# Performance work log

Hardware: AMD Instinct MI355X
Metric: run time of the kernel (lower is better)

## Reference

```python
import jax, jax.numpy as jnp
import numpy as np

N_NODES = 50000
N_EDGES = 1600000
IN_CH = 128
HID_CH = 128


def setup_inputs() -> dict:
    key = jax.random.key(0)
    ks = jax.random.split(key, 8)
    node_embed = jax.random.normal(ks[0], (N_NODES, IN_CH), dtype=jnp.float32)
    node_pos = jax.random.normal(ks[1], (N_NODES, 3), dtype=jnp.float32)
    edge_index = jax.random.randint(ks[2], (2, N_EDGES), 0, N_NODES, dtype=jnp.int64)
    # Linear weights stored as [in, out] so y = x @ W + b (matches torch x @ W.T + b)
    W_res = jax.random.normal(ks[3], (IN_CH, HID_CH), dtype=jnp.float32) / np.sqrt(IN_CH)
    W_msg = jax.random.normal(ks[4], (2 * IN_CH + 1, HID_CH), dtype=jnp.float32) / np.sqrt(2 * IN_CH + 1)
    b_msg = jax.random.normal(ks[5], (HID_CH,), dtype=jnp.float32) * 0.01
    W_upd = jax.random.normal(ks[6], (IN_CH + HID_CH, HID_CH), dtype=jnp.float32) / np.sqrt(IN_CH + HID_CH)
    b_upd = jax.random.normal(ks[7], (HID_CH,), dtype=jnp.float32) * 0.01
    return {"node_embed": node_embed, "node_pos": node_pos, "edge_index": edge_index,
            "W_res": W_res, "W_msg": W_msg, "b_msg": b_msg, "W_upd": W_upd, "b_upd": b_upd}


def reference(node_embed, node_pos, edge_index, W_res, W_msg, b_msg, W_upd, b_upd):
    row, col = edge_index[0], edge_index[1]
    # squared distance per edge: [E, 1]
    diff = node_pos[row] - node_pos[col]
    dist = jnp.sum(diff * diff, axis=1, keepdims=True)
    # message MLP on concat(src, tgt, dist): [E, 2*in+1] -> [E, hidden]
    msg_in = jnp.concatenate([node_embed[row], node_embed[col], dist], axis=-1)
    msg = jax.nn.relu(msg_in @ W_msg + b_msg)
    # scatter-sum messages into target nodes (index = col, as in original)
    aggr = jax.ops.segment_sum(msg, col, num_segments=N_NODES)
    upd_in = jnp.concatenate([node_embed, aggr], axis=-1)
    new_node_embed = node_embed @ W_res + jax.nn.relu(upd_in @ W_upd + b_upd)
    return new_node_embed
```

## Files before the change

kernel.cpp:

```cpp
#include <hip/hip_runtime.h>
#include <hip/hip_bf16.h>
#include <cstdint>


typedef __bf16 bf16x8 __attribute__((ext_vector_type(8)));
typedef float floatx4 __attribute__((ext_vector_type(4)));
typedef float floatx2 __attribute__((ext_vector_type(2)));
typedef unsigned int uintx4 __attribute__((ext_vector_type(4)));

#define BUCKET_CAP 128
#define NBINS 256
#define BIN_CAP 10240
#define PASS2_SPLIT 4

__device__ __forceinline__ ushort f2bf(float f) {
  union { float f; uint i; } v; v.f = f;
  uint r = v.i + 0x7fff + ((v.i >> 16) & 1);
  return (ushort)(r >> 16);
}
__device__ __forceinline__ bf16x8 load_frag(const ushort* p) {
  uint4 v = *(const uint4*)p;
  return __builtin_bit_cast(bf16x8, v);
}
__device__ __forceinline__ floatx2 pmax0(floatx2 a) {
#if __has_builtin(__builtin_elementwise_max)
  return __builtin_elementwise_max(a, (floatx2)(0.f));
#else
  floatx2 r; r.x = fmaxf(a.x, 0.f); r.y = fmaxf(a.y, 0.f); return r;
#endif
}

struct WSrc { const float* s[5]; };

__global__ __launch_bounds__(256) void k0_cast(
    const float* __restrict__ embed, ushort* __restrict__ Eb, int n4, int nb_cast,
    WSrc ws, ushort* __restrict__ Wt)
{
  if ((int)blockIdx.x < nb_cast) {
    int i = blockIdx.x * 256 + threadIdx.x;
    if (i < n4) {
      float4 v = ((const float4*)embed)[i];
      ushort4 o;
      o.x = f2bf(v.x); o.y = f2bf(v.y); o.z = f2bf(v.z); o.w = f2bf(v.w);
      ((ushort4*)Eb)[i] = o;
    }
    return;
  }
  int wb = blockIdx.x - nb_cast;
  const float* s = ws.s[wb];
  ushort* d = Wt + wb * 16384;
  for (int i = threadIdx.x; i < 16384; i += 256) {
    int k = i >> 7, n = i & 127;
    d[n * 128 + k] = f2bf(s[i]);
  }
}

__global__ __launch_bounds__(256) void k1_binpass(
    const int* __restrict__ ei, int E, const float* __restrict__ pos,
    uint* __restrict__ bin_cursor, uint2* __restrict__ binned)
{
  __shared__ uint hist[NBINS];
  __shared__ uint base[NBINS];
  __shared__ uint lcur[NBINS];
  const int t = threadIdx.x;
  hist[t] = 0;
  __syncthreads();

  const int e0 = blockIdx.x * 2048 + t * 8;
  int rr[8], cc[8];
  uint2 rec[8];
  bool any = (e0 < E);
  if (any) {
    int4 r0 = ((const int4*)(ei + e0))[0];
    int4 r1 = ((const int4*)(ei + e0))[1];
    int4 c0 = ((const int4*)(ei + E + e0))[0];
    int4 c1 = ((const int4*)(ei + E + e0))[1];
    rr[0]=r0.x; rr[1]=r0.y; rr[2]=r0.z; rr[3]=r0.w;
    rr[4]=r1.x; rr[5]=r1.y; rr[6]=r1.z; rr[7]=r1.w;
    cc[0]=c0.x; cc[1]=c0.y; cc[2]=c0.z; cc[3]=c0.w;
    cc[4]=c1.x; cc[5]=c1.y; cc[6]=c1.z; cc[7]=c1.w;
#pragma unroll
    for (int j = 0; j < 8; ++j) {
      bool val = (e0 + j < E);
      int r = val ? rr[j] : 0, c = val ? cc[j] : 0;
      float dx = pos[3 * r + 0] - pos[3 * c + 0];
      float dy = pos[3 * r + 1] - pos[3 * c + 1];
      float dz = pos[3 * r + 2] - pos[3 * c + 2];
      float dist = dx * dx + dy * dy + dz * dz;
      rec[j].x = ((uint)c << 16) | (uint)r;
      rec[j].y = (uint)f2bf(dist);
      if (val) atomicAdd(&hist[c >> 8], 1u);
    }
  }
  __syncthreads();
  uint h = hist[t];
  base[t] = h ? atomicAdd(bin_cursor + t, h) : 0u;
  lcur[t] = 0;
  __syncthreads();
  if (any) {
#pragma unroll
    for (int j = 0; j < 8; ++j) {
      if (e0 + j < E) {
        int b = cc[j] >> 8;
        uint ofs = atomicAdd(&lcur[b], 1u);
        uint idx = base[b] + ofs;
        if (idx < BIN_CAP)
          binned[(size_t)b * BIN_CAP + idx] = rec[j];
      }
    }
  }
}

__global__ __launch_bounds__(256) void k2_proj_pass2(
    const ushort* __restrict__ Ab, int M, int rt,
    const ushort* __restrict__ W1t, const ushort* __restrict__ W2t,
    const float* __restrict__ b_msg,
    unsigned char* __restrict__ P1, ushort* __restrict__ P2b,
    const uint* __restrict__ bin_cursor, const uint2* __restrict__ binned,
    int* __restrict__ counts, uint* __restrict__ recs)
{
  if ((int)blockIdx.x >= rt) {
    int b = blockIdx.x - rt;
    int bin = b / PASS2_SPLIT, part = b % PASS2_SPLIT;
    int cnt = (int)min(bin_cursor[bin], (uint)BIN_CAP);
    int s0 = (int)((long)cnt * part / PASS2_SPLIT);
    int s1 = (int)((long)cnt * (part + 1) / PASS2_SPLIT);
    const uint2* src = binned + (size_t)bin * BIN_CAP;
    for (int i = s0 + threadIdx.x; i < s1; i += 256) {
      uint2 rec = src[i];
      uint c = rec.x >> 16;
      int slot = atomicAdd(counts + c, 1);
      if (slot < BUCKET_CAP)
        recs[(size_t)c * BUCKET_CAP + slot] = (rec.x << 16) | (rec.y & 0xffffu);
    }
    return;
  }

  const int wv = threadIdx.x >> 6, lane = threadIdx.x & 63;
  const int q = lane >> 4, lr = lane & 15;
  const int m0 = blockIdx.x * 32;
  const int n0 = wv * 32;

  const ushort* Wt2[2] = {W1t, W2t};
  bf16x8 bfr[2][2][4];
#pragma unroll
  for (int ws = 0; ws < 2; ++ws)
#pragma unroll
    for (int nt = 0; nt < 2; ++nt) {
      int colc = n0 + nt * 16 + lr;
#pragma unroll
      for (int kc = 0; kc < 4; ++kc)
        bfr[ws][nt][kc] = load_frag(Wt2[ws] + colc * 128 + kc * 32 + q * 8);
    }

  floatx4 z = {0.f, 0.f, 0.f, 0.f};
  floatx4 acc[2][2][2];
#pragma unroll
  for (int ws = 0; ws < 2; ++ws)
#pragma unroll
    for (int mt = 0; mt < 2; ++mt)
#pragma unroll
      for (int nt = 0; nt < 2; ++nt) acc[ws][mt][nt] = z;

  const int r0 = min(m0 + lr, M - 1);
  const int r1 = min(m0 + 16 + lr, M - 1);
#pragma unroll
  for (int kc = 0; kc < 4; ++kc) {
    bf16x8 a0 = load_frag(Ab + (size_t)r0 * 128 + kc * 32 + q * 8);
    bf16x8 a1 = load_frag(Ab + (size_t)r1 * 128 + kc * 32 + q * 8);
#pragma unroll
    for (int ws = 0; ws < 2; ++ws)
#pragma unroll
      for (int nt = 0; nt < 2; ++nt) {
        acc[ws][0][nt] = __builtin_amdgcn_mfma_f32_16x16x32_bf16(a0, bfr[ws][nt][kc], acc[ws][0][nt], 0, 0, 0);
        acc[ws][1][nt] = __builtin_amdgcn_mfma_f32_16x16x32_bf16(a1, bfr[ws][nt][kc], acc[ws][1][nt], 0, 0, 0);
      }
  }

#pragma unroll
  for (int nt = 0; nt < 2; ++nt) {
    int colc = n0 + nt * 16 + lr;
    float bias = b_msg[colc];
#pragma unroll
    for (int mt = 0; mt < 2; ++mt)
#pragma unroll
      for (int i = 0; i < 4; ++i) {
        int r = m0 + mt * 16 + q * 4 + i;
        if (r < M) {
          int p8 = __builtin_amdgcn_cvt_pk_fp8_f32(acc[0][mt][nt][i], 0.f, 0, false);
          P1[(size_t)r * 128 + colc] = (unsigned char)(p8 & 0xff);
          P2b[(size_t)r * 128 + colc] = f2bf(acc[1][mt][nt][i] + bias);
        }
      }
  }
}

__global__ __launch_bounds__(256) void aggregate(const int* __restrict__ counts,
                                                 const uint* __restrict__ recs,
                                                 const unsigned char* __restrict__ P1,
                                                 const ushort* __restrict__ P2b,
                                                 const float* __restrict__ wd,
                                                 ushort* __restrict__ aggr, int M)
{
  int n = blockIdx.x * 4 + (threadIdx.x >> 6);
  if (n >= M) return;
  const int lane = threadIdx.x & 63;
  const int ch = lane * 2;

  float2 wl = *(const float2*)(wd + ch);
  floatx2 wv = {wl.x, wl.y};
  uint p2u = *(const uint*)(P2b + (size_t)n * 128 + ch);
  floatx2 p2 = {__int_as_float((int)(p2u << 16)),
                __int_as_float((int)(p2u & 0xffff0000u))};

  const int cnt = min(counts[n], BUCKET_CAP);
  const uint* base = recs + (size_t)n * BUCKET_CAP;
  floatx2 accA = {0.f, 0.f}, accB = {0.f, 0.f};

  auto edge = [&](uint rec, floatx2& acc) {
    float d = __int_as_float((int)(rec << 16));
    uint row = rec >> 16;
    ushort qu = *(const ushort*)(P1 + (size_t)row * 128 + ch);
    floatx2 qv = {__builtin_amdgcn_cvt_f32_fp8((int)qu, 0),
                  __builtin_amdgcn_cvt_f32_fp8((int)qu, 1)};
    floatx2 base2 = qv + p2;
#if __has_builtin(__builtin_elementwise_fma)
    floatx2 t = __builtin_elementwise_fma((floatx2)(d), wv, base2);
#else
    floatx2 t = (floatx2)(d) * wv + base2;
#endif
    acc += pmax0(t);
  };

  int i = 0;
  for (; i + 8 <= cnt; i += 8) {
    uintx4 ra = __builtin_nontemporal_load((const uintx4*)(base + i));
    uintx4 rb = __builtin_nontemporal_load((const uintx4*)(base + i + 4));
    edge(ra.x, accA); edge(ra.y, accB); edge(ra.z, accA); edge(ra.w, accB);
    edge(rb.x, accA); edge(rb.y, accB); edge(rb.z, accA); edge(rb.w, accB);
  }
  for (; i < cnt; ++i) edge(base[i], accA);

  floatx2 acc = accA + accB;
  uint o = (uint)f2bf(acc.x) | ((uint)f2bf(acc.y) << 16);
  *(uint*)(aggr + (size_t)n * 128 + ch) = o;
}

__global__ __launch_bounds__(256) void gemm_upd_mfma(
    const ushort* __restrict__ Eb, const ushort* __restrict__ Gb, int M,
    const ushort* __restrict__ Wu1t, const ushort* __restrict__ Wu2t,
    const ushort* __restrict__ Wrt, const float* __restrict__ b_upd,
    float* __restrict__ out)
{
  const int wv = threadIdx.x >> 6, lane = threadIdx.x & 63;
  const int q = lane >> 4, lr = lane & 15;
  const int m0 = blockIdx.x * 32;
  const int n0 = wv * 32;

  bf16x8 b1[2][4], b2[2][4], br[2][4];
#pragma unroll
  for (int nt = 0; nt < 2; ++nt) {
    int colc = n0 + nt * 16 + lr;
#pragma unroll
    for (int kc = 0; kc < 4; ++kc) {
      b1[nt][kc] = load_frag(Wu1t + colc * 128 + kc * 32 + q * 8);
      b2[nt][kc] = load_frag(Wu2t + colc * 128 + kc * 32 + q * 8);
      br[nt][kc] = load_frag(Wrt  + colc * 128 + kc * 32 + q * 8);
    }
  }

  floatx4 z = {0.f, 0.f, 0.f, 0.f};
  floatx4 acc_u[2][2], acc_r[2][2];
#pragma unroll
  for (int mt = 0; mt < 2; ++mt)
#pragma unroll
    for (int nt = 0; nt < 2; ++nt) { acc_u[mt][nt] = z; acc_r[mt][nt] = z; }

  const int r0 = min(m0 + lr, M - 1);
  const int r1 = min(m0 + 16 + lr, M - 1);
#pragma unroll
  for (int kc = 0; kc < 4; ++kc) {
    bf16x8 ae0 = load_frag(Eb + (size_t)r0 * 128 + kc * 32 + q * 8);
    bf16x8 ae1 = load_frag(Eb + (size_t)r1 * 128 + kc * 32 + q * 8);
    bf16x8 ag0 = load_frag(Gb + (size_t)r0 * 128 + kc * 32 + q * 8);
    bf16x8 ag1 = load_frag(Gb + (size_t)r1 * 128 + kc * 32 + q * 8);
#pragma unroll
    for (int nt = 0; nt < 2; ++nt) {
      acc_u[0][nt] = __builtin_amdgcn_mfma_f32_16x16x32_bf16(ae0, b1[nt][kc], acc_u[0][nt], 0, 0, 0);
      acc_u[1][nt] = __builtin_amdgcn_mfma_f32_16x16x32_bf16(ae1, b1[nt][kc], acc_u[1][nt], 0, 0, 0);
      acc_u[0][nt] = __builtin_amdgcn_mfma_f32_16x16x32_bf16(ag0, b2[nt][kc], acc_u[0][nt], 0, 0, 0);
      acc_u[1][nt] = __builtin_amdgcn_mfma_f32_16x16x32_bf16(ag1, b2[nt][kc], acc_u[1][nt], 0, 0, 0);
      acc_r[0][nt] = __builtin_amdgcn_mfma_f32_16x16x32_bf16(ae0, br[nt][kc], acc_r[0][nt], 0, 0, 0);
      acc_r[1][nt] = __builtin_amdgcn_mfma_f32_16x16x32_bf16(ae1, br[nt][kc], acc_r[1][nt], 0, 0, 0);
    }
  }

#pragma unroll
  for (int nt = 0; nt < 2; ++nt) {
    int colc = n0 + nt * 16 + lr;
    float bias = b_upd[colc];
#pragma unroll
    for (int mt = 0; mt < 2; ++mt)
#pragma unroll
      for (int i = 0; i < 4; ++i) {
        int r = m0 + mt * 16 + q * 4 + i;
        if (r < M)
          out[(size_t)r * 128 + colc] = acc_r[mt][nt][i] + fmaxf(acc_u[mt][nt][i] + bias, 0.f);
      }
  }
}

extern "C" void kernel_launch(void* const* d_in, const int* in_sizes, int n_in,
                              void* d_out, int out_size, void* d_ws, size_t ws_size,
                              hipStream_t stream)
{
  const float* embed = (const float*)d_in[0];
  const float* pos   = (const float*)d_in[1];
  const int*   ei    = (const int*)d_in[2];
  const float* W_res = (const float*)d_in[3];
  const float* W_msg = (const float*)d_in[4];
  const float* b_msg = (const float*)d_in[5];
  const float* W_upd = (const float*)d_in[6];
  const float* b_upd = (const float*)d_in[7];
  float* out = (float*)d_out;

  const int M = in_sizes[0] / 128;
  const int E = in_sizes[2] / 2;

  ushort* Eb = (ushort*)d_ws;
  unsigned char* P1f8 = (unsigned char*)(Eb + (size_t)M * 128);
  ushort* P2b = (ushort*)(P1f8 + (size_t)M * 128);
  ushort* Gb  = P2b + (size_t)M * 128;
  ushort* Wt  = Gb  + (size_t)M * 128;
  uint*   recs = (uint*)(Wt + 5 * 16384);
  uint2*  binned = (uint2*)(recs + (size_t)M * BUCKET_CAP);
  int*    counts = (int*)(binned + (size_t)NBINS * BIN_CAP);
  uint*   bin_cursor = (uint*)(counts + M);

  (void)hipMemsetAsync(counts, 0, (size_t)(M + NBINS) * sizeof(int), stream);

  WSrc wsrc;
  wsrc.s[0] = W_msg;
  wsrc.s[1] = W_msg + 128 * 128;
  wsrc.s[2] = W_res;
  wsrc.s[3] = W_upd;
  wsrc.s[4] = W_upd + 128 * 128;

  int n4 = M * 128 / 4;
  int nb_cast = (n4 + 255) / 256;
  k0_cast<<<nb_cast + 5, 256, 0, stream>>>(embed, Eb, n4, nb_cast, wsrc, Wt);

  int bb = (E + 2047) / 2048;
  k1_binpass<<<bb, 256, 0, stream>>>(ei, E, pos, bin_cursor, binned);

  int rt = (M + 31) / 32;
  k2_proj_pass2<<<rt + NBINS * PASS2_SPLIT, 256, 0, stream>>>(
      Eb, M, rt, Wt, Wt + 16384, b_msg, P1f8, P2b,
      bin_cursor, binned, counts, recs);

  aggregate<<<(M + 3) / 4, 256, 0, stream>>>(counts, recs, P1f8, P2b,
                                             W_msg + 256 * 128, Gb, M);

  gemm_upd_mfma<<<rt, 256, 0, stream>>>(Eb, Gb, M, Wt + 3 * 16384, Wt + 4 * 16384,
                                        Wt + 2 * 16384, b_upd, out);
}
```

Measured before the change: 283.4 us.

## Fuse cast and binning kernels; deepen aggregate unroll with packed fp8 convert

Merges the embedding/weight cast kernel and the edge binning pass into one launch, with block ranges selecting the role, so one kernel launch and its tail go away and the two independent stages can overlap. The aggregate loop now loads 32 records at a time into four accumulators, which gives more gather loads in flight. It also uses a packed fp8-to-f32 convert and computes the row offset with a single shift and mask. The trade-off is higher register pressure in aggregate, and the fused kernel now carries shared memory even for blocks that only cast.

```diff
diff --git a/kernel.cpp b/kernel.cpp
--- a/kernel.cpp
+++ b/kernel.cpp
@@ -29,39 +29,50 @@
   floatx2 r; r.x = fmaxf(a.x, 0.f); r.y = fmaxf(a.y, 0.f); return r;
 #endif
 }
+__device__ __forceinline__ floatx2 cvtpk2(uint qu) {
+#if __has_builtin(__builtin_amdgcn_cvt_pk_f32_fp8)
+  return __builtin_amdgcn_cvt_pk_f32_fp8((int)qu, false);
+#else
+  floatx2 o = {__builtin_amdgcn_cvt_f32_fp8((int)qu, 0),
+               __builtin_amdgcn_cvt_f32_fp8((int)qu, 1)};
+  return o;
+#endif
+}
 
 struct WSrc { const float* s[5]; };
 
-__global__ __launch_bounds__(256) void k0_cast(
+__global__ __launch_bounds__(256) void k01_cast_bin(
     const float* __restrict__ embed, ushort* __restrict__ Eb, int n4, int nb_cast,
-    WSrc ws, ushort* __restrict__ Wt)
-{
-  if ((int)blockIdx.x < nb_cast) {
-    int i = blockIdx.x * 256 + threadIdx.x;
-    if (i < n4) {
-      float4 v = ((const float4*)embed)[i];
-      ushort4 o;
-      o.x = f2bf(v.x); o.y = f2bf(v.y); o.z = f2bf(v.z); o.w = f2bf(v.w);
-      ((ushort4*)Eb)[i] = o;
+    WSrc ws, ushort* __restrict__ Wt,
+    const int* __restrict__ ei, int E, const float* __restrict__ pos,
+    uint* __restrict__ bin_cursor, uint2* __restrict__ binned, int bb)
+{
+  __shared__ uint hist[NBINS];
+  __shared__ uint sbase[NBINS];
+  __shared__ uint lcur[NBINS];
+
+  if ((int)blockIdx.x >= bb) {
+    int cb = blockIdx.x - bb;
+    if (cb < nb_cast) {
+      int i = cb * 256 + threadIdx.x;
+      if (i < n4) {
+        float4 v = ((const float4*)embed)[i];
+        ushort4 o;
+        o.x = f2bf(v.x); o.y = f2bf(v.y); o.z = f2bf(v.z); o.w = f2bf(v.w);
+        ((ushort4*)Eb)[i] = o;
+      }
+      return;
+    }
+    int wb = cb - nb_cast;
+    const float* s = ws.s[wb];
+    ushort* d = Wt + wb * 16384;
+    for (int i = threadIdx.x; i < 16384; i += 256) {
+      int k = i >> 7, n = i & 127;
+      d[n * 128 + k] = f2bf(s[i]);
     }
     return;
   }
-  int wb = blockIdx.x - nb_cast;
-  const float* s = ws.s[wb];
-  ushort* d = Wt + wb * 16384;
-  for (int i = threadIdx.x; i < 16384; i += 256) {
-    int k = i >> 7, n = i & 127;
-    d[n * 128 + k] = f2bf(s[i]);
-  }
-}
-
-__global__ __launch_bounds__(256) void k1_binpass(
-    const int* __restrict__ ei, int E, const float* __restrict__ pos,
-    uint* __restrict__ bin_cursor, uint2* __restrict__ binned)
-{
-  __shared__ uint hist[NBINS];
-  __shared__ uint base[NBINS];
-  __shared__ uint lcur[NBINS];
+
   const int t = threadIdx.x;
   hist[t] = 0;
   __syncthreads();
@@ -94,7 +105,7 @@
   }
   __syncthreads();
   uint h = hist[t];
-  base[t] = h ? atomicAdd(bin_cursor + t, h) : 0u;
+  sbase[t] = h ? atomicAdd(bin_cursor + t, h) : 0u;
   lcur[t] = 0;
   __syncthreads();
   if (any) {
@@ -103,7 +114,7 @@
       if (e0 + j < E) {
         int b = cc[j] >> 8;
         uint ofs = atomicAdd(&lcur[b], 1u);
-        uint idx = base[b] + ofs;
+        uint idx = sbase[b] + ofs;
         if (idx < BIN_CAP)
           binned[(size_t)b * BIN_CAP + idx] = rec[j];
       }
@@ -215,33 +226,53 @@
 
   const int cnt = min(counts[n], BUCKET_CAP);
   const uint* base = recs + (size_t)n * BUCKET_CAP;
-  floatx2 accA = {0.f, 0.f}, accB = {0.f, 0.f};
+
+  floatx2 acc0 = {0.f, 0.f}, acc1 = {0.f, 0.f};
+  floatx2 acc2 = {0.f, 0.f}, acc3 = {0.f, 0.f};
 
   auto edge = [&](uint rec, floatx2& acc) {
     float d = __int_as_float((int)(rec << 16));
-    uint row = rec >> 16;
-    ushort qu = *(const ushort*)(P1 + (size_t)row * 128 + ch);
-    floatx2 qv = {__builtin_amdgcn_cvt_f32_fp8((int)qu, 0),
-                  __builtin_amdgcn_cvt_f32_fp8((int)qu, 1)};
-    floatx2 base2 = qv + p2;
+    uint off = ((rec >> 9) & 0x007fff80u) | (uint)ch;
+    uint qu = (uint)*(const ushort*)(P1 + off);
+    floatx2 s = cvtpk2(qu) + p2;
 #if __has_builtin(__builtin_elementwise_fma)
-    floatx2 t = __builtin_elementwise_fma((floatx2)(d), wv, base2);
+    floatx2 t = __builtin_elementwise_fma((floatx2)(d), wv, s);
 #else
-    floatx2 t = (floatx2)(d) * wv + base2;
+    floatx2 t = (floatx2)(d) * wv + s;
 #endif
     acc += pmax0(t);
   };
 
+  auto do8 = [&](uintx4 a, uintx4 b, floatx2& x, floatx2& y) {
+    edge(a.x, x); edge(a.y, y); edge(a.z, x); edge(a.w, y);
+    edge(b.x, x); edge(b.y, y); edge(b.z, x); edge(b.w, y);
+  };
+
   int i = 0;
+  for (; i + 32 <= cnt; i += 32) {
+    const uintx4* p = (const uintx4*)(base + i);
+    uintx4 v0 = __builtin_nontemporal_load(p + 0);
+    uintx4 v1 = __builtin_nontemporal_load(p + 1);
+    uintx4 v2 = __builtin_nontemporal_load(p + 2);
+    uintx4 v3 = __builtin_nontemporal_load(p + 3);
+    uintx4 v4 = __builtin_nontemporal_load(p + 4);
+    uintx4 v5 = __builtin_nontemporal_load(p + 5);
+    uintx4 v6 = __builtin_nontemporal_load(p + 6);
+    uintx4 v7 = __builtin_nontemporal_load(p + 7);
+    do8(v0, v1, acc0, acc1);
+    do8(v2, v3, acc2, acc3);
+    do8(v4, v5, acc0, acc1);
+    do8(v6, v7, acc2, acc3);
+  }
   for (; i + 8 <= cnt; i += 8) {
-    uintx4 ra = __builtin_nontemporal_load((const uintx4*)(base + i));
-    uintx4 rb = __builtin_nontemporal_load((const uintx4*)(base + i + 4));
-    edge(ra.x, accA); edge(ra.y, accB); edge(ra.z, accA); edge(ra.w, accB);
-    edge(rb.x, accA); edge(rb.y, accB); edge(rb.z, accA); edge(rb.w, accB);
-  }
-  for (; i < cnt; ++i) edge(base[i], accA);
-
-  floatx2 acc = accA + accB;
+    const uintx4* p = (const uintx4*)(base + i);
+    uintx4 v0 = __builtin_nontemporal_load(p + 0);
+    uintx4 v1 = __builtin_nontemporal_load(p + 1);
+    do8(v0, v1, acc0, acc1);
+  }
+  for (; i < cnt; ++i) edge(base[i], acc0);
+
+  floatx2 acc = (acc0 + acc1) + (acc2 + acc3);
   uint o = (uint)f2bf(acc.x) | ((uint)f2bf(acc.y) << 16);
   *(uint*)(aggr + (size_t)n * 128 + ch) = o;
 }
@@ -348,10 +379,9 @@
 
   int n4 = M * 128 / 4;
   int nb_cast = (n4 + 255) / 256;
-  k0_cast<<<nb_cast + 5, 256, 0, stream>>>(embed, Eb, n4, nb_cast, wsrc, Wt);
-
   int bb = (E + 2047) / 2048;
-  k1_binpass<<<bb, 256, 0, stream>>>(ei, E, pos, bin_cursor, binned);
+  k01_cast_bin<<<bb + nb_cast + 5, 256, 0, stream>>>(
+      embed, Eb, n4, nb_cast, wsrc, Wt, ei, E, pos, bin_cursor, binned, bb);
 
   int rt = (M + 31) / 32;
   k2_proj_pass2<<<rt + NBINS * PASS2_SPLIT, 256, 0, stream>>>(
```

Result: slower. 300.8 us (+6.2%).
